# Optimization experiments

Measured on AMD Instinct MI355X. Metric: run time of the kernel, lower is better.

Reference implementation:

```python
import jax, jax.numpy as jnp
import numpy as np


def setup_inputs() -> dict:
    key = jax.random.key(0)
    k1, k2, k3, k4 = jax.random.split(key, 4)
    B, T, K, N = 8, 16, 4096, 16384
    x = jax.random.normal(k1, (B, T, K), dtype=jnp.float32)
    # int8 weights in [-127, 127]
    weight_int8 = jax.random.randint(k2, (N, K), -127, 128, dtype=jnp.int32).astype(jnp.int8)
    # row-wise absmax scales (positive)
    weight_scales = jax.random.uniform(k3, (N,), dtype=jnp.float32, minval=0.1, maxval=2.0)
    bias = jax.random.normal(k4, (N,), dtype=jnp.float32)
    return {"x": x, "weight_int8": weight_int8, "weight_scales": weight_scales, "bias": bias}


def reference(x, weight_int8, weight_scales, bias):
    # dequantize_rowwise: W_fp = int8 * (scale / 127) per output row
    w = weight_int8.astype(x.dtype) * (weight_scales / 127.0).astype(x.dtype)[:, None]  # [N, K]
    # F.linear(x, w, bias) = x @ w.T + bias
    out = jnp.einsum('btk,nk->btn', x, w) + bias
    return out
```

## Files before the change

kernel.cpp:

```cpp
#include <hip/hip_runtime.h>
#include <hip/hip_bf16.h>

typedef __attribute__((ext_vector_type(8))) short short8;
typedef __attribute__((ext_vector_type(4))) float f32x4;
typedef __attribute__((ext_vector_type(4))) int   i32x4;

#define KD 4096
#define ND 16384
#define MD 128

__device__ __forceinline__ ushort f2bf_rn(float f) {
    unsigned u = __float_as_uint(f);
    u += 0x7FFFu + ((u >> 16) & 1u);
    return (ushort)(u >> 16);
}

__device__ __forceinline__ ushort i2bf(int v) {
    return (ushort)(__float_as_uint((float)v) >> 16);
}

__global__ __launch_bounds__(256) void pack_x_kernel(const float* __restrict__ x,
                                                     ushort* __restrict__ xp) {
    int tid  = blockIdx.x * 256 + threadIdx.x;
    int lane = tid & 63;
    int mt   = (tid >> 6) & 7;
    int kb   = tid >> 9;
    int m = (mt << 4) + (lane & 15);
    int k = (kb << 5) + ((lane >> 4) << 3);
    const f32x4* src = reinterpret_cast<const f32x4*>(x + (size_t)m * KD + k);
    f32x4 a = src[0];
    f32x4 b = src[1];
    short8 v;
    v[0] = (short)f2bf_rn(a[0]); v[1] = (short)f2bf_rn(a[1]);
    v[2] = (short)f2bf_rn(a[2]); v[3] = (short)f2bf_rn(a[3]);
    v[4] = (short)f2bf_rn(b[0]); v[5] = (short)f2bf_rn(b[1]);
    v[6] = (short)f2bf_rn(b[2]); v[7] = (short)f2bf_rn(b[3]);
    *reinterpret_cast<short8*>(xp + (size_t)tid * 8) = v;
}

#define GLOAD_LDS16(g, l)                                                        \
    __builtin_amdgcn_global_load_lds((const __attribute__((address_space(1))) void*)(g), \
                                     (__attribute__((address_space(3))) void*)(l), 16, 0, 0)

__global__ __launch_bounds__(256, 2) void gemm_kernel(const int* __restrict__ wgt,
                                                      const ushort* __restrict__ xp,
                                                      const float* __restrict__ scales,
                                                      const float* __restrict__ bias,
                                                      float* __restrict__ out) {
    __shared__ __align__(16) char lds[49152];

    const int tid  = threadIdx.x;
    const int lane = tid & 63;
    const int w    = tid >> 6;
    const int nb   = blockIdx.x & 255;
    const int h    = blockIdx.x >> 8;
    const int n0   = nb << 6;
    const int cl   = lane & 15;
    const int cq   = lane >> 4;

    const char* asrc = (const char*)xp + (h << 12) + (w << 10) + (lane << 4);

    const int* wsrc0;
    const int* wsrc1;
    const int* wsrc2;
    const int* wsrc3;
    {
        int c0 = (w << 4) + 0  + cq;
        int c1 = (w << 4) + 4  + cq;
        int c2 = (w << 4) + 8  + cq;
        int c3 = (w << 4) + 12 + cq;
        wsrc0 = wgt + (size_t)(n0 + c0) * KD + ((cl ^ (c0 & 7)) << 2);
        wsrc1 = wgt + (size_t)(n0 + c1) * KD + ((cl ^ (c1 & 7)) << 2);
        wsrc2 = wgt + (size_t)(n0 + c2) * KD + ((cl ^ (c2 & 7)) << 2);
        wsrc3 = wgt + (size_t)(n0 + c3) * KD + ((cl ^ (c3 & 7)) << 2);
    }

    f32x4 acc[4];
#pragma unroll
    for (int i = 0; i < 4; ++i) acc[i] = (f32x4){0.f, 0.f, 0.f, 0.f};

    char* dA = lds + (w << 10);
    char* dW = lds + 16384 + (w << 12);

#define STAGE(t, b) do {                                                        \
        const char* _as = asrc + (size_t)(t) * 16384;                           \
        GLOAD_LDS16(_as,        dA + (b) * 8192);                               \
        GLOAD_LDS16(_as + 8192, dA + (b) * 8192 + 4096);                        \
        const int _k0 = (t) * 64;                                               \
        GLOAD_LDS16(wsrc0 + _k0, dW + (b) * 16384);                             \
        GLOAD_LDS16(wsrc1 + _k0, dW + (b) * 16384 + 1024);                      \
        GLOAD_LDS16(wsrc2 + _k0, dW + (b) * 16384 + 2048);                      \
        GLOAD_LDS16(wsrc3 + _k0, dW + (b) * 16384 + 3072);                      \
    } while (0)

    const char* rA = lds + (lane << 4);
    const char* rW = lds + 16384 + (((w << 4) + cl) << 8);
    const int sw   = (cl & 7) << 4;
    const int q32  = cq << 5;

#define COMPUTE(b) do {                                                         \
        _Pragma("unroll")                                                       \
        for (int _kbl = 0; _kbl < 2; ++_kbl) {                                  \
            int _ib = ((_kbl << 7) + q32) ^ sw;                                 \
            i32x4 _lo = *reinterpret_cast<const i32x4*>(rW + (b) * 16384 + _ib);        \
            i32x4 _hi = *reinterpret_cast<const i32x4*>(rW + (b) * 16384 + (_ib ^ 16)); \
            short8 _bf;                                                         \
            _bf[0] = (short)i2bf(_lo[0]); _bf[1] = (short)i2bf(_lo[1]);         \
            _bf[2] = (short)i2bf(_lo[2]); _bf[3] = (short)i2bf(_lo[3]);         \
            _bf[4] = (short)i2bf(_hi[0]); _bf[5] = (short)i2bf(_hi[1]);         \
            _bf[6] = (short)i2bf(_hi[2]); _bf[7] = (short)i2bf(_hi[3]);         \
            const char* _ab = rA + (b) * 8192 + _kbl * 4096;                    \
            _Pragma("unroll")                                                   \
            for (int _m = 0; _m < 4; ++_m) {                                    \
                short8 _af = *reinterpret_cast<const short8*>(_ab + _m * 1024); \
                acc[_m] = __builtin_amdgcn_mfma_f32_16x16x32_bf16(_af, _bf, acc[_m], 0, 0, 0); \
            }                                                                   \
        }                                                                       \
    } while (0)

    STAGE(0, 0);
    __syncthreads();
    for (int t = 0; t < 63; ++t) {
        const int cb = t & 1;
        STAGE(t + 1, cb ^ 1);
        COMPUTE(cb);
        __syncthreads();
    }
    COMPUTE(1);

    const int ncol = n0 + (w << 4) + cl;
    const float s  = scales[ncol] * (1.0f / 127.0f);
    const float bv = bias[ncol];
    const int rb = cq << 2;
#pragma unroll
    for (int m = 0; m < 4; ++m) {
#pragma unroll
        for (int r = 0; r < 4; ++r) {
            int mg = (h << 6) + (m << 4) + rb + r;
            out[(size_t)mg * ND + ncol] = acc[m][r] * s + bv;
        }
    }
#undef STAGE
#undef COMPUTE
}

extern "C" void kernel_launch(void* const* d_in, const int* in_sizes, int n_in,
                              void* d_out, int out_size, void* d_ws, size_t ws_size,
                              hipStream_t stream) {
    const float* x      = (const float*)d_in[0];
    const int*   wgt    = (const int*)d_in[1];
    const float* scales = (const float*)d_in[2];
    const float* bias   = (const float*)d_in[3];
    float* out = (float*)d_out;
    ushort* xp = (ushort*)d_ws;

    pack_x_kernel<<<MD * KD / (8 * 256), 256, 0, stream>>>(x, xp);
    gemm_kernel<<<512, 256, 0, stream>>>(wgt, xp, scales, bias, out);
}
```

Measured before the change: 68.93 us.

## Replace direct global-to-LDS loads with register-staged two-deep prefetch pipeline

Swaps the global_load_lds async copies for ordinary global loads into registers, two tiles ahead, followed by explicit LDS stores after each compute step. The barrier now waits only on LDS counters, so global loads for tile t+2 can stay in flight across the barrier. The goal is deeper prefetch to hide HBM latency on the memory-bound int8 weight stream. In exchange it uses 12 more vector registers per thread, adds LDS store instructions, and may hurt occupancy at 2 blocks per CU.

```diff
diff --git a/kernel.cpp b/kernel.cpp
--- a/kernel.cpp
+++ b/kernel.cpp
@@ -38,9 +38,10 @@
     *reinterpret_cast<short8*>(xp + (size_t)tid * 8) = v;
 }
 
-#define GLOAD_LDS16(g, l)                                                        \
-    __builtin_amdgcn_global_load_lds((const __attribute__((address_space(1))) void*)(g), \
-                                     (__attribute__((address_space(3))) void*)(l), 16, 0, 0)
+#define BARRIER() do {                                                          \
+        asm volatile("s_waitcnt lgkmcnt(0)" ::: "memory");                      \
+        __builtin_amdgcn_s_barrier();                                           \
+    } while (0)
 
 __global__ __launch_bounds__(256, 2) void gemm_kernel(const int* __restrict__ wgt,
                                                       const ushort* __restrict__ xp,
@@ -59,7 +60,6 @@
     const int cq   = lane >> 4;
 
     const char* asrc = (const char*)xp + (h << 12) + (w << 10) + (lane << 4);
-
     const int* wsrc0;
     const int* wsrc1;
     const int* wsrc2;
@@ -75,22 +75,34 @@
         wsrc3 = wgt + (size_t)(n0 + c3) * KD + ((cl ^ (c3 & 7)) << 2);
     }
 
+    char* wAp = lds + (w << 10) + (lane << 4);
+    char* wWp = lds + 16384 + (w << 12) + (lane << 4);
+
     f32x4 acc[4];
 #pragma unroll
     for (int i = 0; i < 4; ++i) acc[i] = (f32x4){0.f, 0.f, 0.f, 0.f};
 
-    char* dA = lds + (w << 10);
-    char* dW = lds + 16384 + (w << 12);
+    i32x4 SAa0, SAa1, SAw0, SAw1, SAw2, SAw3;
+    i32x4 SBa0, SBa1, SBw0, SBw1, SBw2, SBw3;
 
-#define STAGE(t, b) do {                                                        \
+#define LOADSET(S, t) do {                                                      \
         const char* _as = asrc + (size_t)(t) * 16384;                           \
-        GLOAD_LDS16(_as,        dA + (b) * 8192);                               \
-        GLOAD_LDS16(_as + 8192, dA + (b) * 8192 + 4096);                        \
+        S##a0 = *reinterpret_cast<const i32x4*>(_as);                           \
+        S##a1 = *reinterpret_cast<const i32x4*>(_as + 8192);                    \
         const int _k0 = (t) * 64;                                               \
-        GLOAD_LDS16(wsrc0 + _k0, dW + (b) * 16384);                             \
-        GLOAD_LDS16(wsrc1 + _k0, dW + (b) * 16384 + 1024);                      \
-        GLOAD_LDS16(wsrc2 + _k0, dW + (b) * 16384 + 2048);                      \
-        GLOAD_LDS16(wsrc3 + _k0, dW + (b) * 16384 + 3072);                      \
+        S##w0 = *reinterpret_cast<const i32x4*>(wsrc0 + _k0);                   \
+        S##w1 = *reinterpret_cast<const i32x4*>(wsrc1 + _k0);                   \
+        S##w2 = *reinterpret_cast<const i32x4*>(wsrc2 + _k0);                   \
+        S##w3 = *reinterpret_cast<const i32x4*>(wsrc3 + _k0);                   \
+    } while (0)
+
+#define WRITESET(S, b) do {                                                     \
+        *reinterpret_cast<i32x4*>(wAp + (b) * 8192)         = S##a0;            \
+        *reinterpret_cast<i32x4*>(wAp + (b) * 8192 + 4096)  = S##a1;            \
+        *reinterpret_cast<i32x4*>(wWp + (b) * 16384)        = S##w0;            \
+        *reinterpret_cast<i32x4*>(wWp + (b) * 16384 + 1024) = S##w1;            \
+        *reinterpret_cast<i32x4*>(wWp + (b) * 16384 + 2048) = S##w2;            \
+        *reinterpret_cast<i32x4*>(wWp + (b) * 16384 + 3072) = S##w3;            \
     } while (0)
 
     const char* rA = lds + (lane << 4);
@@ -118,14 +130,27 @@
         }                                                                       \
     } while (0)
 
-    STAGE(0, 0);
-    __syncthreads();
-    for (int t = 0; t < 63; ++t) {
-        const int cb = t & 1;
-        STAGE(t + 1, cb ^ 1);
-        COMPUTE(cb);
-        __syncthreads();
+    LOADSET(SA, 0);
+    LOADSET(SB, 1);
+    WRITESET(SA, 0);
+    BARRIER();
+
+#pragma unroll 1
+    for (int t = 0; t < 62; t += 2) {
+        LOADSET(SA, t + 2);
+        COMPUTE(0);
+        WRITESET(SB, 1);
+        BARRIER();
+
+        LOADSET(SB, t + 3);
+        COMPUTE(1);
+        WRITESET(SA, 0);
+        BARRIER();
     }
+
+    COMPUTE(0);
+    WRITESET(SB, 1);
+    BARRIER();
     COMPUTE(1);
 
     const int ncol = n0 + (w << 4) + cl;
@@ -140,7 +165,8 @@
             out[(size_t)mg * ND + ncol] = acc[m][r] * s + bv;
         }
     }
-#undef STAGE
+#undef LOADSET
+#undef WRITESET
 #undef COMPUTE
 }
 
```

New measurement: 87.48 us. +26.9%, slower.

## Load activations directly to registers and double the K-tile per stage

Applied to the files above, without the earlier changes.

Activation fragments now go from global memory straight into registers, each wave fetching its own copy, instead of being staged through LDS. Only the int8 weights go through LDS, and each stage covers 128 K values instead of 64, which halves the number of barriers. LDS use grows to 64KB and 16 short8 registers per thread are added, which may limit occupancy. Each wave now issues its own global loads of the same activation data, so there are redundant loads, though they are likely served from L2.

```diff
diff --git a/kernel.cpp b/kernel.cpp
--- a/kernel.cpp
+++ b/kernel.cpp
@@ -47,7 +47,7 @@
                                                       const float* __restrict__ scales,
                                                       const float* __restrict__ bias,
                                                       float* __restrict__ out) {
-    __shared__ __align__(16) char lds[49152];
+    __shared__ __align__(16) char lds[65536];
 
     const int tid  = threadIdx.x;
     const int lane = tid & 63;
@@ -58,74 +58,77 @@
     const int cl   = lane & 15;
     const int cq   = lane >> 4;
 
-    const char* asrc = (const char*)xp + (h << 12) + (w << 10) + (lane << 4);
+    const char* axbase = (const char*)xp + (h << 12) + (lane << 4);
 
-    const int* wsrc0;
-    const int* wsrc1;
-    const int* wsrc2;
-    const int* wsrc3;
-    {
-        int c0 = (w << 4) + 0  + cq;
-        int c1 = (w << 4) + 4  + cq;
-        int c2 = (w << 4) + 8  + cq;
-        int c3 = (w << 4) + 12 + cq;
-        wsrc0 = wgt + (size_t)(n0 + c0) * KD + ((cl ^ (c0 & 7)) << 2);
-        wsrc1 = wgt + (size_t)(n0 + c1) * KD + ((cl ^ (c1 & 7)) << 2);
-        wsrc2 = wgt + (size_t)(n0 + c2) * KD + ((cl ^ (c2 & 7)) << 2);
-        wsrc3 = wgt + (size_t)(n0 + c3) * KD + ((cl ^ (c3 & 7)) << 2);
+    const int l5  = lane >> 5;
+    const int l31 = lane & 31;
+    const int* wsrc[8];
+#pragma unroll
+    for (int i = 0; i < 8; ++i) {
+        int c = (w << 4) + (i << 1) + l5;
+        int koff = (l31 << 2) ^ ((c & 7) << 2);
+        wsrc[i] = wgt + (size_t)(n0 + c) * KD + koff;
     }
 
     f32x4 acc[4];
 #pragma unroll
     for (int i = 0; i < 4; ++i) acc[i] = (f32x4){0.f, 0.f, 0.f, 0.f};
 
-    char* dA = lds + (w << 10);
-    char* dW = lds + 16384 + (w << 12);
+    short8 afr[16];
+
+    char* dW = lds + (w << 13);
 
 #define STAGE(t, b) do {                                                        \
-        const char* _as = asrc + (size_t)(t) * 16384;                           \
-        GLOAD_LDS16(_as,        dA + (b) * 8192);                               \
-        GLOAD_LDS16(_as + 8192, dA + (b) * 8192 + 4096);                        \
-        const int _k0 = (t) * 64;                                               \
-        GLOAD_LDS16(wsrc0 + _k0, dW + (b) * 16384);                             \
-        GLOAD_LDS16(wsrc1 + _k0, dW + (b) * 16384 + 1024);                      \
-        GLOAD_LDS16(wsrc2 + _k0, dW + (b) * 16384 + 2048);                      \
-        GLOAD_LDS16(wsrc3 + _k0, dW + (b) * 16384 + 3072);                      \
+        char* _d = dW + (b) * 32768;                                            \
+        _Pragma("unroll")                                                       \
+        for (int _i = 0; _i < 8; ++_i)                                          \
+            GLOAD_LDS16(wsrc[_i] + (t) * 128, _d + _i * 1024);                  \
     } while (0)
 
-    const char* rA = lds + (lane << 4);
-    const char* rW = lds + 16384 + (((w << 4) + cl) << 8);
-    const int sw   = (cl & 7) << 4;
-    const int q32  = cq << 5;
+#define ALOAD(t) do {                                                           \
+        const char* _ax = axbase + (size_t)(t) * 32768;                         \
+        _Pragma("unroll")                                                       \
+        for (int _q = 0; _q < 4; ++_q)                                          \
+            _Pragma("unroll")                                                   \
+            for (int _kb = 0; _kb < 4; ++_kb)                                   \
+                afr[_q * 4 + _kb] = *reinterpret_cast<const short8*>(           \
+                    _ax + _kb * 8192 + _q * 1024);                              \
+    } while (0)
+
+    const char* rW = lds + (((w << 4) + cl) << 9);
+    const unsigned sw  = (unsigned)((cl & 7) << 4);
+    const unsigned q32 = (unsigned)(cq << 5);
 
 #define COMPUTE(b) do {                                                         \
+        const char* _wc = rW + (b) * 32768;                                     \
         _Pragma("unroll")                                                       \
-        for (int _kbl = 0; _kbl < 2; ++_kbl) {                                  \
-            int _ib = ((_kbl << 7) + q32) ^ sw;                                 \
-            i32x4 _lo = *reinterpret_cast<const i32x4*>(rW + (b) * 16384 + _ib);        \
-            i32x4 _hi = *reinterpret_cast<const i32x4*>(rW + (b) * 16384 + (_ib ^ 16)); \
+        for (int _kb = 0; _kb < 4; ++_kb) {                                     \
+            unsigned _off = (unsigned)((_kb << 7) + q32) ^ sw;                  \
+            i32x4 _lo = *reinterpret_cast<const i32x4*>(_wc + _off);            \
+            i32x4 _hi = *reinterpret_cast<const i32x4*>(_wc + (_off ^ 16u));    \
             short8 _bf;                                                         \
             _bf[0] = (short)i2bf(_lo[0]); _bf[1] = (short)i2bf(_lo[1]);         \
             _bf[2] = (short)i2bf(_lo[2]); _bf[3] = (short)i2bf(_lo[3]);         \
             _bf[4] = (short)i2bf(_hi[0]); _bf[5] = (short)i2bf(_hi[1]);         \
             _bf[6] = (short)i2bf(_hi[2]); _bf[7] = (short)i2bf(_hi[3]);         \
-            const char* _ab = rA + (b) * 8192 + _kbl * 4096;                    \
-            _Pragma("unroll")                                                   \
-            for (int _m = 0; _m < 4; ++_m) {                                    \
-                short8 _af = *reinterpret_cast<const short8*>(_ab + _m * 1024); \
-                acc[_m] = __builtin_amdgcn_mfma_f32_16x16x32_bf16(_af, _bf, acc[_m], 0, 0, 0); \
-            }                                                                   \
+            acc[0] = __builtin_amdgcn_mfma_f32_16x16x32_bf16(afr[0 * 4 + _kb], _bf, acc[0], 0, 0, 0); \
+            acc[1] = __builtin_amdgcn_mfma_f32_16x16x32_bf16(afr[1 * 4 + _kb], _bf, acc[1], 0, 0, 0); \
+            acc[2] = __builtin_amdgcn_mfma_f32_16x16x32_bf16(afr[2 * 4 + _kb], _bf, acc[2], 0, 0, 0); \
+            acc[3] = __builtin_amdgcn_mfma_f32_16x16x32_bf16(afr[3 * 4 + _kb], _bf, acc[3], 0, 0, 0); \
         }                                                                       \
     } while (0)
 
     STAGE(0, 0);
     __syncthreads();
-    for (int t = 0; t < 63; ++t) {
-        const int cb = t & 1;
-        STAGE(t + 1, cb ^ 1);
-        COMPUTE(cb);
+#pragma unroll 1
+    for (int t = 0; t < 31; ++t) {
+        ALOAD(t);
+        __builtin_amdgcn_sched_barrier(0);
+        STAGE(t + 1, (t + 1) & 1);
+        COMPUTE(t & 1);
         __syncthreads();
     }
+    ALOAD(31);
     COMPUTE(1);
 
     const int ncol = n0 + (w << 4) + cl;
@@ -141,6 +144,7 @@
         }
     }
 #undef STAGE
+#undef ALOAD
 #undef COMPUTE
 }
 
```

Result: slower. 95.00 us (+37.8%).

## Warp-specialize GEMM with producer waves and triple-buffered LDS pipeline

Applied to the files above, without the earlier changes.

Splits each 512-thread block into four producer waves that issue global-to-LDS loads and four consumer waves that run MFMAs, using a three-stage LDS ring buffer synchronized by barriers. Each block now covers all 128 rows for its 64 columns, so the weight tile is read once instead of twice across the two M-halves. The aim is to halve weight traffic and hide load latency behind compute. In exchange there is one block per CU with 96KB LDS, a 256-block grid that underfills the CUs, and more accumulator registers per consumer.

```diff
diff --git a/kernel.cpp b/kernel.cpp
--- a/kernel.cpp
+++ b/kernel.cpp
@@ -42,106 +42,125 @@
     __builtin_amdgcn_global_load_lds((const __attribute__((address_space(1))) void*)(g), \
                                      (__attribute__((address_space(3))) void*)(l), 16, 0, 0)
 
-__global__ __launch_bounds__(256, 2) void gemm_kernel(const int* __restrict__ wgt,
-                                                      const ushort* __restrict__ xp,
-                                                      const float* __restrict__ scales,
-                                                      const float* __restrict__ bias,
-                                                      float* __restrict__ out) {
-    __shared__ __align__(16) char lds[49152];
+__global__ __launch_bounds__(512) void gemm_kernel(const int* __restrict__ wgt,
+                                                   const ushort* __restrict__ xp,
+                                                   const float* __restrict__ scales,
+                                                   const float* __restrict__ bias,
+                                                   float* __restrict__ out) {
+    __shared__ __align__(16) char lds[98304];
 
     const int tid  = threadIdx.x;
     const int lane = tid & 63;
     const int w    = tid >> 6;
-    const int nb   = blockIdx.x & 255;
-    const int h    = blockIdx.x >> 8;
-    const int n0   = nb << 6;
+    const int n0   = blockIdx.x << 6;
     const int cl   = lane & 15;
     const int cq   = lane >> 4;
 
-    const char* asrc = (const char*)xp + (h << 12) + (w << 10) + (lane << 4);
+    if (w >= 4) {
+        const int p = w - 4;
+        const char* asrc = (const char*)xp + (p << 12) + (lane << 4);
+        const int* wsrc0;
+        const int* wsrc1;
+        const int* wsrc2;
+        const int* wsrc3;
+        {
+            int c0 = (p << 4) + 0  + cq;
+            int c1 = (p << 4) + 4  + cq;
+            int c2 = (p << 4) + 8  + cq;
+            int c3 = (p << 4) + 12 + cq;
+            wsrc0 = wgt + (size_t)(n0 + c0) * KD + ((cl ^ (c0 & 7)) << 2);
+            wsrc1 = wgt + (size_t)(n0 + c1) * KD + ((cl ^ (c1 & 7)) << 2);
+            wsrc2 = wgt + (size_t)(n0 + c2) * KD + ((cl ^ (c2 & 7)) << 2);
+            wsrc3 = wgt + (size_t)(n0 + c3) * KD + ((cl ^ (c3 & 7)) << 2);
+        }
+        char* dA = lds + (p << 12);
+        char* dW = lds + 49152 + (p << 12);
 
-    const int* wsrc0;
-    const int* wsrc1;
-    const int* wsrc2;
-    const int* wsrc3;
-    {
-        int c0 = (w << 4) + 0  + cq;
-        int c1 = (w << 4) + 4  + cq;
-        int c2 = (w << 4) + 8  + cq;
-        int c3 = (w << 4) + 12 + cq;
-        wsrc0 = wgt + (size_t)(n0 + c0) * KD + ((cl ^ (c0 & 7)) << 2);
-        wsrc1 = wgt + (size_t)(n0 + c1) * KD + ((cl ^ (c1 & 7)) << 2);
-        wsrc2 = wgt + (size_t)(n0 + c2) * KD + ((cl ^ (c2 & 7)) << 2);
-        wsrc3 = wgt + (size_t)(n0 + c3) * KD + ((cl ^ (c3 & 7)) << 2);
+#define STAGE(t, b) do {                                                        \
+            const char* _as = asrc + (size_t)(t) * 16384;                       \
+            char* _dA = dA + (b) * 16384;                                       \
+            GLOAD_LDS16(_as,        _dA);                                       \
+            GLOAD_LDS16(_as + 1024, _dA + 1024);                                \
+            GLOAD_LDS16(_as + 2048, _dA + 2048);                                \
+            GLOAD_LDS16(_as + 3072, _dA + 3072);                                \
+            const int _k0 = (t) * 64;                                           \
+            char* _dW = dW + (b) * 16384;                                       \
+            GLOAD_LDS16(wsrc0 + _k0, _dW);                                      \
+            GLOAD_LDS16(wsrc1 + _k0, _dW + 1024);                               \
+            GLOAD_LDS16(wsrc2 + _k0, _dW + 2048);                               \
+            GLOAD_LDS16(wsrc3 + _k0, _dW + 3072);                               \
+        } while (0)
+
+        STAGE(0, 0);
+        STAGE(1, 1);
+        asm volatile("s_waitcnt vmcnt(8)" ::: "memory");
+        __builtin_amdgcn_s_barrier();
+
+        int b2 = 2;
+#pragma unroll 1
+        for (int t = 0; t < 64; ++t) {
+            if (t + 2 < 64) {
+                STAGE(t + 2, b2);
+                asm volatile("s_waitcnt vmcnt(8)" ::: "memory");
+            } else if (t + 1 < 64) {
+                asm volatile("s_waitcnt vmcnt(0)" ::: "memory");
+            }
+            __builtin_amdgcn_s_barrier();
+            b2 = (b2 == 2) ? 0 : b2 + 1;
+        }
+#undef STAGE
+        return;
     }
 
-    f32x4 acc[4];
+    f32x4 acc[8];
 #pragma unroll
-    for (int i = 0; i < 4; ++i) acc[i] = (f32x4){0.f, 0.f, 0.f, 0.f};
-
-    char* dA = lds + (w << 10);
-    char* dW = lds + 16384 + (w << 12);
-
-#define STAGE(t, b) do {                                                        \
-        const char* _as = asrc + (size_t)(t) * 16384;                           \
-        GLOAD_LDS16(_as,        dA + (b) * 8192);                               \
-        GLOAD_LDS16(_as + 8192, dA + (b) * 8192 + 4096);                        \
-        const int _k0 = (t) * 64;                                               \
-        GLOAD_LDS16(wsrc0 + _k0, dW + (b) * 16384);                             \
-        GLOAD_LDS16(wsrc1 + _k0, dW + (b) * 16384 + 1024);                      \
-        GLOAD_LDS16(wsrc2 + _k0, dW + (b) * 16384 + 2048);                      \
-        GLOAD_LDS16(wsrc3 + _k0, dW + (b) * 16384 + 3072);                      \
-    } while (0)
+    for (int i = 0; i < 8; ++i) acc[i] = (f32x4){0.f, 0.f, 0.f, 0.f};
 
     const char* rA = lds + (lane << 4);
-    const char* rW = lds + 16384 + (((w << 4) + cl) << 8);
-    const int sw   = (cl & 7) << 4;
-    const int q32  = cq << 5;
+    const char* rW = lds + 49152 + (((w << 4) + cl) << 8);
+    const unsigned sw  = (unsigned)((cl & 7) << 4);
+    const unsigned q32 = (unsigned)(cq << 5);
 
-#define COMPUTE(b) do {                                                         \
-        _Pragma("unroll")                                                       \
-        for (int _kbl = 0; _kbl < 2; ++_kbl) {                                  \
-            int _ib = ((_kbl << 7) + q32) ^ sw;                                 \
-            i32x4 _lo = *reinterpret_cast<const i32x4*>(rW + (b) * 16384 + _ib);        \
-            i32x4 _hi = *reinterpret_cast<const i32x4*>(rW + (b) * 16384 + (_ib ^ 16)); \
-            short8 _bf;                                                         \
-            _bf[0] = (short)i2bf(_lo[0]); _bf[1] = (short)i2bf(_lo[1]);         \
-            _bf[2] = (short)i2bf(_lo[2]); _bf[3] = (short)i2bf(_lo[3]);         \
-            _bf[4] = (short)i2bf(_hi[0]); _bf[5] = (short)i2bf(_hi[1]);         \
-            _bf[6] = (short)i2bf(_hi[2]); _bf[7] = (short)i2bf(_hi[3]);         \
-            const char* _ab = rA + (b) * 8192 + _kbl * 4096;                    \
-            _Pragma("unroll")                                                   \
-            for (int _m = 0; _m < 4; ++_m) {                                    \
-                short8 _af = *reinterpret_cast<const short8*>(_ab + _m * 1024); \
-                acc[_m] = __builtin_amdgcn_mfma_f32_16x16x32_bf16(_af, _bf, acc[_m], 0, 0, 0); \
-            }                                                                   \
-        }                                                                       \
-    } while (0)
+    __syncthreads();
 
-    STAGE(0, 0);
-    __syncthreads();
-    for (int t = 0; t < 63; ++t) {
-        const int cb = t & 1;
-        STAGE(t + 1, cb ^ 1);
-        COMPUTE(cb);
+    int bc = 0;
+#pragma unroll 1
+    for (int t = 0; t < 64; ++t) {
+        const char* wb = rW + bc * 16384;
+        const char* ab = rA + bc * 16384;
+#pragma unroll
+        for (int j = 0; j < 2; ++j) {
+            unsigned off = (unsigned)((j << 7) + q32) ^ sw;
+            i32x4 lo = *reinterpret_cast<const i32x4*>(wb + off);
+            i32x4 hi = *reinterpret_cast<const i32x4*>(wb + (off ^ 16u));
+            short8 bf;
+            bf[0] = (short)i2bf(lo[0]); bf[1] = (short)i2bf(lo[1]);
+            bf[2] = (short)i2bf(lo[2]); bf[3] = (short)i2bf(lo[3]);
+            bf[4] = (short)i2bf(hi[0]); bf[5] = (short)i2bf(hi[1]);
+            bf[6] = (short)i2bf(hi[2]); bf[7] = (short)i2bf(hi[3]);
+            const char* aj = ab + j * 8192;
+#pragma unroll
+            for (int mt = 0; mt < 8; ++mt) {
+                short8 af = *reinterpret_cast<const short8*>(aj + mt * 1024);
+                acc[mt] = __builtin_amdgcn_mfma_f32_16x16x32_bf16(af, bf, acc[mt], 0, 0, 0);
+            }
+        }
         __syncthreads();
+        bc = (bc == 2) ? 0 : bc + 1;
     }
-    COMPUTE(1);
 
     const int ncol = n0 + (w << 4) + cl;
     const float s  = scales[ncol] * (1.0f / 127.0f);
     const float bv = bias[ncol];
     const int rb = cq << 2;
 #pragma unroll
-    for (int m = 0; m < 4; ++m) {
+    for (int mt = 0; mt < 8; ++mt) {
 #pragma unroll
         for (int r = 0; r < 4; ++r) {
-            int mg = (h << 6) + (m << 4) + rb + r;
-            out[(size_t)mg * ND + ncol] = acc[m][r] * s + bv;
+            int mg = (mt << 4) + rb + r;
+            out[(size_t)mg * ND + ncol] = acc[mt][r] * s + bv;
         }
     }
-#undef STAGE
-#undef COMPUTE
 }
 
 extern "C" void kernel_launch(void* const* d_in, const int* in_sizes, int n_in,
@@ -155,5 +174,5 @@
     ushort* xp = (ushort*)d_ws;
 
     pack_x_kernel<<<MD * KD / (8 * 256), 256, 0, stream>>>(x, xp);
-    gemm_kernel<<<512, 256, 0, stream>>>(wgt, xp, scales, bias, out);
+    gemm_kernel<<<256, 512, 0, stream>>>(wgt, xp, scales, bias, out);
 }
```

After: 57.77 us (median of 2 runs). 1.19x faster.
